# Kernel optimization log

Measured on AMD Instinct MI355X. Metric: run time of the kernel, lower is better.

The kernel has to match this reference:

```python
import jax, jax.numpy as jnp
import numpy as np

DIM = 96; HEADS = 3; HEAD_DIM = 32; INNER = HEADS * HEAD_DIM; MLP = 384
WS = 4; WV = WS ** 3; SHIFT = WS // 2  # displacement = window//2
SPATIAL = 64


def _rel_indices():
    c = np.stack(np.meshgrid(np.arange(WS), np.arange(WS), np.arange(WS), indexing='ij'), -1).reshape(-1, 3)
    return c[:, None] - c[None, :] + (WS - 1)  # [WV, WV, 3] in [0, 2*WS-2]

REL = _rel_indices()


def _make_mask():
    # standard Swin shifted-window mask: label contiguity regions, partition, -inf cross-region
    X = Y = Z = SPATIAL
    lab = np.zeros((X, Y, Z), np.int32); cnt = 0
    sl = (slice(0, -WS), slice(-WS, -SHIFT), slice(-SHIFT, None))
    for sx in sl:
        for sy in sl:
            for sz in sl:
                lab[sx, sy, sz] = cnt; cnt += 1
    n = X // WS
    lab = lab.reshape(n, WS, n, WS, n, WS).transpose(0, 2, 4, 1, 3, 5).reshape(-1, WV)
    m = np.where(lab[:, :, None] != lab[:, None, :], -1e9, 0.0).astype(np.float32)
    return jnp.asarray(m)  # [nW, WV, WV]

MASK = _make_mask()


def _ln(x, g, b):
    m = x.mean(-1, keepdims=True)
    v = ((x - m) ** 2).mean(-1, keepdims=True)
    return (x - m) * jax.lax.rsqrt(v + 1e-5) * g + b


def _window_attn(x, W_qkv, W_out, b_out, pos_tab):
    B, X, Y, Z, _ = x.shape
    x = jnp.roll(x, (-SHIFT, -SHIFT, -SHIFT), axis=(1, 2, 3))  # cyclic shift
    qkv = x @ W_qkv  # [B,X,Y,Z,3*INNER]
    nx, ny, nz = X // WS, Y // WS, Z // WS
    qkv = qkv.reshape(B, nx, WS, ny, WS, nz, WS, 3, HEADS, HEAD_DIM)
    qkv = qkv.transpose(7, 0, 8, 1, 3, 5, 2, 4, 6, 9).reshape(3, B, HEADS, nx * ny * nz, WV, HEAD_DIM)
    q, k, v = qkv[0], qkv[1], qkv[2]
    dots = jnp.einsum('bhwid,bhwjd->bhwij', q, k) * (HEAD_DIM ** -0.5)
    bias = pos_tab[REL[..., 0], REL[..., 1], REL[..., 2]]  # [WV,WV]
    dots = dots + bias + MASK[None, None]
    attn = jax.nn.softmax(dots, axis=-1)
    out = jnp.einsum('bhwij,bhwjd->bhwid', attn, v)
    out = out.reshape(B, HEADS, nx, ny, nz, WS, WS, WS, HEAD_DIM)
    out = out.transpose(0, 2, 5, 3, 6, 4, 7, 1, 8).reshape(B, X, Y, Z, INNER)
    out = out @ W_out + b_out
    return jnp.roll(out, (SHIFT, SHIFT, SHIFT), axis=(1, 2, 3))  # cyclic back-shift


def setup_inputs() -> dict:
    key = jax.random.key(0)
    ks = jax.random.split(key, 8)
    w = lambda k, shape, s=0.02: (jax.random.normal(k, shape, jnp.float32) * s)
    return {
        'x': jax.random.normal(ks[0], (1, SPATIAL, SPATIAL, SPATIAL, DIM), jnp.float32),
        'W_qkv': w(ks[1], (DIM, 3 * INNER)),
        'W_out': w(ks[2], (INNER, DIM)),
        'b_out': jnp.zeros((DIM,), jnp.float32),
        'pos_tab': w(ks[3], (2 * WS - 1, 2 * WS - 1, 2 * WS - 1), 1.0),
        'ln1_g': jnp.ones((DIM,), jnp.float32), 'ln1_b': jnp.zeros((DIM,), jnp.float32),
        'ln2_g': jnp.ones((DIM,), jnp.float32), 'ln2_b': jnp.zeros((DIM,), jnp.float32),
        'W1': w(ks[4], (DIM, MLP)), 'b1': jnp.zeros((MLP,), jnp.float32),
        'W2': w(ks[5], (MLP, DIM)), 'b2': jnp.zeros((DIM,), jnp.float32),
    }


def reference(x, W_qkv, W_out, b_out, pos_tab, ln1_g, ln1_b, ln2_g, ln2_b, W1, b1, W2, b2):
    # Residual(PreNorm(WindowAttention3D))
    x = x + _window_attn(_ln(x, ln1_g, ln1_b), W_qkv, W_out, b_out, pos_tab)
    # Residual(PreNorm(FeedForward3D)): Linear -> GELU -> Linear (dropout=0)
    h = _ln(x, ln2_g, ln2_b)
    h = jax.nn.gelu(h @ W1 + b1, approximate=False) @ W2 + b2
    return x + h
```

## Files before the change

### kernel.cpp

```cpp
#include <hip/hip_runtime.h>
#include <hip/hip_bf16.h>

typedef __attribute__((ext_vector_type(8))) short bf16x8;
typedef __attribute__((ext_vector_type(4))) short s16x4;
typedef __attribute__((ext_vector_type(4))) float f32x4;

#define NWIN 4096

__device__ __forceinline__ unsigned short f2bf(float f) {
    __hip_bfloat16 h = __float2bfloat16(f);
    unsigned short u;
    __builtin_memcpy(&u, &h, 2);
    return u;
}
__device__ __forceinline__ float bf2f(unsigned short u) {
    return __uint_as_float(((unsigned int)u) << 16);
}
__device__ __forceinline__ int region(int g) { return (g >= 60) + (g >= 62); }

__global__ void convert_weights(const float* __restrict__ Wqkv, const float* __restrict__ Wout,
                                const float* __restrict__ W1, const float* __restrict__ W2,
                                unsigned short* __restrict__ wq_t, unsigned short* __restrict__ wo_t,
                                unsigned short* __restrict__ w1_t, unsigned short* __restrict__ w2_t) {
    int idx = blockIdx.x * blockDim.x + threadIdx.x;
    if (idx < 27648) {
        int n = idx / 96, k = idx % 96;
        wq_t[idx] = f2bf(Wqkv[k * 288 + n]);
    } else if (idx < 27648 + 9216) {
        int i = idx - 27648; int n = i / 96, k = i % 96;
        wo_t[i] = f2bf(Wout[k * 96 + n]);
    } else if (idx < 27648 + 9216 + 36864) {
        int i = idx - 36864; int n = i / 96, k = i % 96;
        w1_t[i] = f2bf(W1[k * 384 + n]);
    } else if (idx < 110592) {
        int i = idx - 73728; int n = i / 384, k = i % 384;
        w2_t[i] = f2bf(W2[k * 96 + n]);
    }
}

__global__ __launch_bounds__(384, 4) void ln_qkv_attn_kernel(
    const float* __restrict__ x,
    const float* __restrict__ ln1_g, const float* __restrict__ ln1_b,
    const unsigned short* __restrict__ wq_t,
    const float* __restrict__ pos_tab,
    unsigned short* __restrict__ a_out)
{
    __shared__ __align__(16) unsigned short SH[22272];
    __shared__ __align__(16) float posl[344];
    unsigned short* q_s = SH;
    unsigned short* k_s = SH + 7680;
    unsigned short* vT  = SH + 15360;
    unsigned short* y_s = SH + 15360;
    unsigned short* P_s = SH;

    int win = blockIdx.x;
    int tid = threadIdx.x;
    int w = tid >> 6, lane = tid & 63, lr = lane & 15, kh = lane >> 4;
    int ix = win >> 8, iy = (win >> 4) & 15, iz = win & 15;

    if (tid < 343) posl[tid] = pos_tab[tid];

    {
        int grp = tid >> 4, gi = tid & 15;
        float gv[6], bv[6];
        #pragma unroll
        for (int j = 0; j < 6; ++j) { gv[j] = ln1_g[gi + 16 * j]; bv[j] = ln1_b[gi + 16 * j]; }
        #pragma unroll
        for (int p = 0; p < 3; ++p) {
            int t = grp + p * 24;
            if (t < 64) {
                int wx = t >> 4, wy = (t >> 2) & 3, wz = t & 3;
                int sx = (ix * 4 + wx + 2) & 63, sy = (iy * 4 + wy + 2) & 63, sz = (iz * 4 + wz + 2) & 63;
                const float* src = x + ((size_t)((sx * 64 + sy) * 64 + sz)) * 96;
                float v[6]; float s = 0.f, sq = 0.f;
                #pragma unroll
                for (int j = 0; j < 6; ++j) { v[j] = src[gi + 16 * j]; s += v[j]; sq += v[j] * v[j]; }
                #pragma unroll
                for (int m = 8; m >= 1; m >>= 1) { s += __shfl_xor(s, m, 16); sq += __shfl_xor(sq, m, 16); }
                float mean = s * (1.0f / 96.0f);
                float var = sq * (1.0f / 96.0f) - mean * mean;
                float rstd = rsqrtf(var + 1e-5f);
                #pragma unroll
                for (int j = 0; j < 6; ++j)
                    y_s[t * 104 + gi + 16 * j] = f2bf((v[j] - mean) * rstd * gv[j] + bv[j]);
            }
        }
    }
    __syncthreads();

    f32x4 acc3[4][3];
    {
        #pragma unroll
        for (int m = 0; m < 4; ++m)
            #pragma unroll
            for (int n = 0; n < 3; ++n) acc3[m][n] = (f32x4){0.f, 0.f, 0.f, 0.f};
        #pragma unroll
        for (int ks = 0; ks < 3; ++ks) {
            int k0 = ks * 32;
            bf16x8 a[4], bb[3];
            #pragma unroll
            for (int m = 0; m < 4; ++m)
                a[m] = *(const bf16x8*)&y_s[(m * 16 + lr) * 104 + k0 + kh * 8];
            #pragma unroll
            for (int n = 0; n < 3; ++n)
                bb[n] = *(const bf16x8*)(wq_t + (size_t)(w * 48 + n * 16 + lr) * 96 + k0 + kh * 8);
            #pragma unroll
            for (int m = 0; m < 4; ++m)
                #pragma unroll
                for (int n = 0; n < 3; ++n)
                    acc3[m][n] = __builtin_amdgcn_mfma_f32_16x16x32_bf16(a[m], bb[n], acc3[m][n], 0, 0, 0);
        }
    }
    __syncthreads();

    {
        const float scale = 0.17677669529663689f;
        #pragma unroll
        for (int n = 0; n < 3; ++n) {
            int base = w * 48 + n * 16;
            int qq = base / 96, cc0 = base % 96;
            int hh = cc0 >> 5, d0 = cc0 & 31;
            if (qq == 2) {
                #pragma unroll
                for (int m = 0; m < 4; ++m) {
                    s16x4 pv;
                    #pragma unroll
                    for (int r = 0; r < 4; ++r) pv[r] = (short)f2bf(acc3[m][n][r]);
                    *(s16x4*)&vT[(hh * 32 + d0 + lr) * 72 + m * 16 + kh * 4] = pv;
                }
            } else {
                unsigned short* dst = (qq == 0) ? q_s : k_s;
                float sc = (qq == 0) ? scale : 1.0f;
                #pragma unroll
                for (int m = 0; m < 4; ++m)
                    #pragma unroll
                    for (int r = 0; r < 4; ++r) {
                        int tok = m * 16 + kh * 4 + r;
                        dst[(hh * 64 + tok) * 40 + d0 + lr] = f2bf(acc3[m][n][r] * sc);
                    }
            }
        }
    }
    __syncthreads();

    int h3 = w >> 1, rb = (w & 1) * 32;
    f32x4 sa[2][4];
    {
        bf16x8 aq[2], bk[4];
        #pragma unroll
        for (int mm = 0; mm < 2; ++mm)
            aq[mm] = *(const bf16x8*)&q_s[(h3 * 64 + rb + mm * 16 + lr) * 40 + kh * 8];
        #pragma unroll
        for (int n = 0; n < 4; ++n)
            bk[n] = *(const bf16x8*)&k_s[(h3 * 64 + n * 16 + lr) * 40 + kh * 8];
        #pragma unroll
        for (int mm = 0; mm < 2; ++mm)
            #pragma unroll
            for (int n = 0; n < 4; ++n)
                sa[mm][n] = __builtin_amdgcn_mfma_f32_16x16x32_bf16(aq[mm], bk[n], (f32x4){0.f,0.f,0.f,0.f}, 0, 0, 0);

        int labj[4], jwx[4], jwy[4], jwz[4];
        #pragma unroll
        for (int n = 0; n < 4; ++n) {
            int j = n * 16 + lr;
            jwx[n] = j >> 4; jwy[n] = (j >> 2) & 3; jwz[n] = j & 3;
            labj[n] = 9 * region(ix * 4 + jwx[n]) + 3 * region(iy * 4 + jwy[n]) + region(iz * 4 + jwz[n]);
        }
        #pragma unroll
        for (int mm = 0; mm < 2; ++mm)
            #pragma unroll
            for (int r = 0; r < 4; ++r) {
                int i = rb + mm * 16 + kh * 4 + r;
                int iwx = i >> 4, iwy = (i >> 2) & 3, iwz = i & 3;
                int labi = 9 * region(ix * 4 + iwx) + 3 * region(iy * 4 + iwy) + region(iz * 4 + iwz);
                #pragma unroll
                for (int n = 0; n < 4; ++n) {
                    float bias = posl[((iwx - jwx[n] + 3) * 7 + (iwy - jwy[n] + 3)) * 7 + (iwz - jwz[n] + 3)];
                    sa[mm][n][r] += bias + (labi != labj[n] ? -1e9f : 0.0f);
                }
                float mx = fmaxf(fmaxf(sa[mm][0][r], sa[mm][1][r]), fmaxf(sa[mm][2][r], sa[mm][3][r]));
                #pragma unroll
                for (int s = 1; s < 16; s <<= 1) mx = fmaxf(mx, __shfl_xor(mx, s, 16));
                float e0 = __expf(sa[mm][0][r] - mx), e1 = __expf(sa[mm][1][r] - mx);
                float e2 = __expf(sa[mm][2][r] - mx), e3 = __expf(sa[mm][3][r] - mx);
                float sum = e0 + e1 + e2 + e3;
                #pragma unroll
                for (int s = 1; s < 16; s <<= 1) sum += __shfl_xor(sum, s, 16);
                float rs = 1.0f / sum;
                sa[mm][0][r] = e0 * rs; sa[mm][1][r] = e1 * rs;
                sa[mm][2][r] = e2 * rs; sa[mm][3][r] = e3 * rs;
            }
    }
    __syncthreads();

    #pragma unroll
    for (int mm = 0; mm < 2; ++mm)
        #pragma unroll
        for (int n = 0; n < 4; ++n)
            #pragma unroll
            for (int r = 0; r < 4; ++r)
                P_s[(h3 * 64 + rb + mm * 16 + kh * 4 + r) * 72 + n * 16 + lr] = f2bf(sa[mm][n][r]);
    __syncthreads();

    {
        f32x4 oa[2][2];
        #pragma unroll
        for (int mm = 0; mm < 2; ++mm)
            #pragma unroll
            for (int n = 0; n < 2; ++n) oa[mm][n] = (f32x4){0.f, 0.f, 0.f, 0.f};
        #pragma unroll
        for (int ks = 0; ks < 2; ++ks) {
            int k0 = ks * 32;
            bf16x8 ap[2], bv[2];
            #pragma unroll
            for (int mm = 0; mm < 2; ++mm)
                ap[mm] = *(const bf16x8*)&P_s[(h3 * 64 + rb + mm * 16 + lr) * 72 + k0 + kh * 8];
            #pragma unroll
            for (int n = 0; n < 2; ++n)
                bv[n] = *(const bf16x8*)&vT[(h3 * 32 + n * 16 + lr) * 72 + k0 + kh * 8];
            #pragma unroll
            for (int mm = 0; mm < 2; ++mm)
                #pragma unroll
                for (int n = 0; n < 2; ++n)
                    oa[mm][n] = __builtin_amdgcn_mfma_f32_16x16x32_bf16(ap[mm], bv[n], oa[mm][n], 0, 0, 0);
        }
        #pragma unroll
        for (int mm = 0; mm < 2; ++mm)
            #pragma unroll
            for (int n = 0; n < 2; ++n)
                #pragma unroll
                for (int r = 0; r < 4; ++r) {
                    int tok = rb + mm * 16 + kh * 4 + r;
                    a_out[((size_t)win * 64 + tok) * 96 + h3 * 32 + n * 16 + lr] = f2bf(oa[mm][n][r]);
                }
    }
}

__global__ __launch_bounds__(256, 4) void proj_mlp5_kernel(
    const unsigned short* __restrict__ a_out,
    const unsigned short* __restrict__ wo_t, const float* __restrict__ b_out,
    const float* __restrict__ x,
    const float* __restrict__ g2, const float* __restrict__ bt2,
    const unsigned short* __restrict__ w1_t, const float* __restrict__ b1,
    const unsigned short* __restrict__ w2_t, const float* __restrict__ b2,
    float* __restrict__ out)
{
    __shared__ __align__(16) unsigned short SH[13312];
    unsigned short* xl = SH;
    unsigned short* gl = SH + 6656;
    float* tile = (float*)SH;

    int win = blockIdx.x;
    int tid = threadIdx.x;
    int w = tid >> 6, lane = tid & 63, lr = lane & 15, kh = lane >> 4;
    int ix = win >> 8, iy = (win >> 4) & 15, iz = win & 15;
    int tb = w * 16;

    int px = (ix * 4 + w + 2) & 63;
    int py = (iy * 4 + kh + 2) & 63;
    int rowbase = (px * 64 + py) * 64;
    int o[4];
    #pragma unroll
    for (int r = 0; r < 4; ++r) o[r] = (rowbase + ((iz * 4 + r + 2) & 63)) * 96;

    float x1v[6][4];
    {
        f32x4 pa[6];
        #pragma unroll
        for (int n = 0; n < 6; ++n) pa[n] = (f32x4){0.f, 0.f, 0.f, 0.f};
        #pragma unroll
        for (int ks = 0; ks < 3; ++ks) {
            int k0 = ks * 32;
            bf16x8 a = *(const bf16x8*)(a_out + ((size_t)win * 64 + tb + lr) * 96 + k0 + kh * 8);
            #pragma unroll
            for (int n = 0; n < 6; ++n) {
                bf16x8 bb = *(const bf16x8*)(wo_t + (size_t)(n * 16 + lr) * 96 + k0 + kh * 8);
                pa[n] = __builtin_amdgcn_mfma_f32_16x16x32_bf16(a, bb, pa[n], 0, 0, 0);
            }
        }
        #pragma unroll
        for (int n = 0; n < 6; ++n) {
            int c = n * 16 + lr;
            float bo = b_out[c];
            #pragma unroll
            for (int r = 0; r < 4; ++r)
                x1v[n][r] = x[o[r] + c] + pa[n][r] + bo;
        }
        float g2c[6], bc2[6];
        #pragma unroll
        for (int n = 0; n < 6; ++n) { g2c[n] = g2[n * 16 + lr]; bc2[n] = bt2[n * 16 + lr]; }
        #pragma unroll
        for (int r = 0; r < 4; ++r) {
            float s = 0.f, sq = 0.f;
            #pragma unroll
            for (int n = 0; n < 6; ++n) { s += x1v[n][r]; sq += x1v[n][r] * x1v[n][r]; }
            #pragma unroll
            for (int m = 8; m >= 1; m >>= 1) { s += __shfl_xor(s, m, 16); sq += __shfl_xor(sq, m, 16); }
            float mean = s * (1.0f / 96.0f);
            float var = sq * (1.0f / 96.0f) - mean * mean;
            float rstd = rsqrtf(var + 1e-5f);
            int t = tb + kh * 4 + r;
            #pragma unroll
            for (int n = 0; n < 6; ++n)
                xl[t * 104 + n * 16 + lr] = f2bf((x1v[n][r] - mean) * rstd * g2c[n] + bc2[n]);
        }
    }
    __syncthreads();

    int wm = w & 1, wn = w >> 1;
    f32x4 acc2[2][3];
    #pragma unroll
    for (int mf = 0; mf < 2; ++mf)
        #pragma unroll
        for (int nf = 0; nf < 3; ++nf) acc2[mf][nf] = (f32x4){0.f, 0.f, 0.f, 0.f};

    for (int ch = 0; ch < 4; ++ch) {
        f32x4 a1[2][3];
        #pragma unroll
        for (int mf = 0; mf < 2; ++mf)
            #pragma unroll
            for (int nf = 0; nf < 3; ++nf) a1[mf][nf] = (f32x4){0.f, 0.f, 0.f, 0.f};
        #pragma unroll
        for (int ks = 0; ks < 3; ++ks) {
            int k0 = ks * 32;
            bf16x8 af[2], bfr[3];
            #pragma unroll
            for (int mf = 0; mf < 2; ++mf)
                af[mf] = *(const bf16x8*)&xl[(wm * 32 + mf * 16 + lr) * 104 + k0 + kh * 8];
            #pragma unroll
            for (int nf = 0; nf < 3; ++nf)
                bfr[nf] = *(const bf16x8*)(w1_t + (size_t)(ch * 96 + wn * 48 + nf * 16 + lr) * 96 + k0 + kh * 8);
            #pragma unroll
            for (int mf = 0; mf < 2; ++mf)
                #pragma unroll
                for (int nf = 0; nf < 3; ++nf)
                    a1[mf][nf] = __builtin_amdgcn_mfma_f32_16x16x32_bf16(af[mf], bfr[nf], a1[mf][nf], 0, 0, 0);
        }
        #pragma unroll
        for (int nf = 0; nf < 3; ++nf) {
            int lcol = wn * 48 + nf * 16 + lr;
            float bias = b1[ch * 96 + lcol];
            #pragma unroll
            for (int mf = 0; mf < 2; ++mf)
                #pragma unroll
                for (int r = 0; r < 4; ++r) {
                    float u = a1[mf][nf][r] + bias;
                    float t = 1.5957691216057308f * (u + 0.044715f * u * u * u);
                    float ge = u * __builtin_amdgcn_rcpf(1.0f + __expf(-t));
                    gl[(wm * 32 + mf * 16 + kh * 4 + r) * 104 + lcol] = f2bf(ge);
                }
        }
        __syncthreads();
        #pragma unroll
        for (int kc = 0; kc < 3; ++kc) {
            int k0 = kc * 32;
            bf16x8 ag[2];
            #pragma unroll
            for (int mf = 0; mf < 2; ++mf)
                ag[mf] = *(const bf16x8*)&gl[(wm * 32 + mf * 16 + lr) * 104 + k0 + kh * 8];
            #pragma unroll
            for (int nf = 0; nf < 3; ++nf) {
                bf16x8 bb = *(const bf16x8*)(w2_t + (size_t)(wn * 48 + nf * 16 + lr) * 384 + ch * 96 + k0 + kh * 8);
                #pragma unroll
                for (int mf = 0; mf < 2; ++mf)
                    acc2[mf][nf] = __builtin_amdgcn_mfma_f32_16x16x32_bf16(ag[mf], bb, acc2[mf][nf], 0, 0, 0);
            }
        }
        __syncthreads();
    }

    #pragma unroll
    for (int r = 0; r < 4; ++r) {
        int t = tb + kh * 4 + r;
        #pragma unroll
        for (int n = 0; n < 6; ++n)
            tile[t * 100 + n * 16 + lr] = x1v[n][r];
    }
    __syncthreads();
    #pragma unroll
    for (int nf = 0; nf < 3; ++nf) {
        int col = wn * 48 + nf * 16 + lr;
        float bc = b2[col];
        #pragma unroll
        for (int mf = 0; mf < 2; ++mf)
            #pragma unroll
            for (int r = 0; r < 4; ++r) {
                int row = wm * 32 + mf * 16 + kh * 4 + r;
                tile[row * 100 + col] += acc2[mf][nf][r] + bc;
            }
    }
    __syncthreads();
    #pragma unroll
    for (int j = 0; j < 6; ++j) {
        int f4 = j * 256 + tid;
        int token = f4 / 24, c4 = f4 % 24;
        int wx = token >> 4, wy = (token >> 2) & 3, wz = token & 3;
        int qx = (ix * 4 + wx + 2) & 63, qy = (iy * 4 + wy + 2) & 63, qz = (iz * 4 + wz + 2) & 63;
        size_t g = ((size_t)((qx * 64 + qy) * 64 + qz)) * 96 + c4 * 4;
        f32x4 v = *(const f32x4*)&tile[token * 100 + c4 * 4];
        *(f32x4*)&out[g] = v;
    }
}

extern "C" void kernel_launch(void* const* d_in, const int* in_sizes, int n_in,
                              void* d_out, int out_size, void* d_ws, size_t ws_size,
                              hipStream_t stream) {
    const float* x       = (const float*)d_in[0];
    const float* Wqkv    = (const float*)d_in[1];
    const float* Wout    = (const float*)d_in[2];
    const float* b_out   = (const float*)d_in[3];
    const float* pos_tab = (const float*)d_in[4];
    const float* ln1_g   = (const float*)d_in[5];
    const float* ln1_b   = (const float*)d_in[6];
    const float* ln2_g   = (const float*)d_in[7];
    const float* ln2_b   = (const float*)d_in[8];
    const float* W1      = (const float*)d_in[9];
    const float* b1      = (const float*)d_in[10];
    const float* W2      = (const float*)d_in[11];
    const float* b2      = (const float*)d_in[12];
    float* out = (float*)d_out;

    char* ws = (char*)d_ws;
    unsigned short* a_out = (unsigned short*)(ws);
    unsigned short* wq_t  = (unsigned short*)(ws + 50331648);
    unsigned short* wo_t  = wq_t + 27648;
    unsigned short* w1_t  = wo_t + 9216;
    unsigned short* w2_t  = w1_t + 36864;

    convert_weights<<<432, 256, 0, stream>>>(Wqkv, Wout, W1, W2, wq_t, wo_t, w1_t, w2_t);
    ln_qkv_attn_kernel<<<NWIN, 384, 0, stream>>>(x, ln1_g, ln1_b, wq_t, pos_tab, a_out);
    proj_mlp5_kernel<<<NWIN, 256, 0, stream>>>(a_out, wo_t, b_out, x,
                                               ln2_g, ln2_b, w1_t, b1, w2_t, b2, out);
}
```

Measured before the change: 231.4 us.

## Process two windows per block in projection+MLP kernel to reuse weight fragments

The fused out-projection, LayerNorm and MLP kernel now handles two attention windows per 512-thread block instead of one window per 256-thread block. The MLP GEMMs work on a 128-row tile, with four warps along M and two along N, so each W1/W2 fragment load is shared by twice as many tokens, halving weight traffic per window. Shared memory doubles to about 53 KB per block. That may cap resident blocks per CU, and larger blocks mean coarser synchronisation. The store loop is rewritten with incremental index stepping to cover both windows.

```diff
diff --git a/kernel.cpp b/kernel.cpp
--- a/kernel.cpp
+++ b/kernel.cpp
@@ -236,7 +236,7 @@
     }
 }
 
-__global__ __launch_bounds__(256, 4) void proj_mlp5_kernel(
+__global__ __launch_bounds__(512, 4) void proj_mlp6_kernel(
     const unsigned short* __restrict__ a_out,
     const unsigned short* __restrict__ wo_t, const float* __restrict__ b_out,
     const float* __restrict__ x,
@@ -245,18 +245,21 @@
     const unsigned short* __restrict__ w2_t, const float* __restrict__ b2,
     float* __restrict__ out)
 {
-    __shared__ __align__(16) unsigned short SH[13312];
+    __shared__ __align__(16) unsigned short SH[26624];
     unsigned short* xl = SH;
-    unsigned short* gl = SH + 6656;
+    unsigned short* gl = SH + 13312;
     float* tile = (float*)SH;
 
-    int win = blockIdx.x;
     int tid = threadIdx.x;
     int w = tid >> 6, lane = tid & 63, lr = lane & 15, kh = lane >> 4;
+    int wh = w >> 2;
+    int wl = w & 3;
+    int win = blockIdx.x * 2 + wh;
     int ix = win >> 8, iy = (win >> 4) & 15, iz = win & 15;
-    int tb = w * 16;
-
-    int px = (ix * 4 + w + 2) & 63;
+    int tb = wl * 16;
+    int row0 = w * 16;
+
+    int px = (ix * 4 + wl + 2) & 63;
     int py = (iy * 4 + kh + 2) & 63;
     int rowbase = (px * 64 + py) * 64;
     int o[4];
@@ -299,7 +302,7 @@
             float mean = s * (1.0f / 96.0f);
             float var = sq * (1.0f / 96.0f) - mean * mean;
             float rstd = rsqrtf(var + 1e-5f);
-            int t = tb + kh * 4 + r;
+            int t = row0 + kh * 4 + r;
             #pragma unroll
             for (int n = 0; n < 6; ++n)
                 xl[t * 104 + n * 16 + lr] = f2bf((x1v[n][r] - mean) * rstd * g2c[n] + bc2[n]);
@@ -307,7 +310,7 @@
     }
     __syncthreads();
 
-    int wm = w & 1, wn = w >> 1;
+    int wm = w & 3, wn = w >> 2;
     f32x4 acc2[2][3];
     #pragma unroll
     for (int mf = 0; mf < 2; ++mf)
@@ -371,7 +374,7 @@
 
     #pragma unroll
     for (int r = 0; r < 4; ++r) {
-        int t = tb + kh * 4 + r;
+        int t = row0 + kh * 4 + r;
         #pragma unroll
         for (int n = 0; n < 6; ++n)
             tile[t * 100 + n * 16 + lr] = x1v[n][r];
@@ -390,15 +393,22 @@
             }
     }
     __syncthreads();
-    #pragma unroll
-    for (int j = 0; j < 6; ++j) {
-        int f4 = j * 256 + tid;
-        int token = f4 / 24, c4 = f4 % 24;
-        int wx = token >> 4, wy = (token >> 2) & 3, wz = token & 3;
-        int qx = (ix * 4 + wx + 2) & 63, qy = (iy * 4 + wy + 2) & 63, qz = (iz * 4 + wz + 2) & 63;
-        size_t g = ((size_t)((qx * 64 + qy) * 64 + qz)) * 96 + c4 * 4;
-        f32x4 v = *(const f32x4*)&tile[token * 100 + c4 * 4];
-        *(f32x4*)&out[g] = v;
+    {
+        int token = tid / 24;
+        int c4 = tid - token * 24;
+        #pragma unroll
+        for (int j = 0; j < 6; ++j) {
+            int wf = blockIdx.x * 2 + (token >> 6);
+            int tok = token & 63;
+            int fx = wf >> 8, fy = (wf >> 4) & 15, fz = wf & 15;
+            int wx = tok >> 4, wy = (tok >> 2) & 3, wz = tok & 3;
+            int qx = (fx * 4 + wx + 2) & 63, qy = (fy * 4 + wy + 2) & 63, qz = (fz * 4 + wz + 2) & 63;
+            size_t g = ((size_t)((qx * 64 + qy) * 64 + qz)) * 96 + c4 * 4;
+            f32x4 v = *(const f32x4*)&tile[token * 100 + c4 * 4];
+            *(f32x4*)&out[g] = v;
+            token += 21; c4 += 8;
+            if (c4 >= 24) { c4 -= 24; token += 1; }
+        }
     }
 }
 
@@ -429,6 +439,6 @@
 
     convert_weights<<<432, 256, 0, stream>>>(Wqkv, Wout, W1, W2, wq_t, wo_t, w1_t, w2_t);
     ln_qkv_attn_kernel<<<NWIN, 384, 0, stream>>>(x, ln1_g, ln1_b, wq_t, pos_tab, a_out);
-    proj_mlp5_kernel<<<NWIN, 256, 0, stream>>>(a_out, wo_t, b_out, x,
-                                               ln2_g, ln2_b, w1_t, b1, w2_t, b2, out);
-}
+    proj_mlp6_kernel<<<NWIN / 2, 512, 0, stream>>>(a_out, wo_t, b_out, x,
+                                                   ln2_g, ln2_b, w1_t, b1, w2_t, b2, out);
+}
```

After: 245.9 us. +6.3%, slower.
